# Performance work log

Hardware: AMD Instinct MI355X
Metric: run time of the kernel (lower is better)

Reference implementation:

```python
import jax, jax.numpy as jnp
import numpy as np

B, T, C = 4, 2048, 1024
H = 16
D = C // H  # 64

def setup_inputs() -> dict:
    key = jax.random.key(0)
    k1, k2, k3, k4, k5 = jax.random.split(key, 5)
    s = 0.02
    return {
        "x": jax.random.normal(k1, (B, T, C), dtype=jnp.float32),
        "Wqkv": jax.random.normal(k2, (C, 3 * C), dtype=jnp.float32) * s,
        "bqkv": jnp.zeros((3 * C,), dtype=jnp.float32),
        "Wout": jax.random.normal(k3, (C, C), dtype=jnp.float32) * s,
        "bout": jnp.zeros((C,), dtype=jnp.float32),
    }

def reference(x, Wqkv, bqkv, Wout, bout):
    b, t, c = x.shape
    scale = D ** -0.5
    qkv = x @ Wqkv + bqkv                      # [B,T,3C]
    qkv = qkv.reshape(b, t, 3, H, D)
    q = qkv[:, :, 0].transpose(0, 2, 1, 3)     # [B,H,T,D]
    k = qkv[:, :, 1].transpose(0, 2, 1, 3)
    v = qkv[:, :, 2].transpose(0, 2, 1, 3)
    att = jnp.einsum('bhqd,bhkd->bhqk', q, k) * scale
    causal = jnp.tril(jnp.ones((t, t), dtype=bool))
    att = jnp.where(causal, att, -jnp.inf)
    att = jax.nn.softmax(att, axis=-1)
    y = jnp.einsum('bhqk,bhkd->bhqd', att, v)  # [B,H,T,D]
    y = y.transpose(0, 2, 1, 3).reshape(b, t, c)
    return y @ Wout + bout
```

## Files before the change

kernel.cpp:

```cpp
#include <hip/hip_runtime.h>
#include <hip/hip_bf16.h>


using f32x4 = __attribute__((ext_vector_type(4))) float;
using s16x8 = __attribute__((ext_vector_type(8))) short;
using s16x4 = __attribute__((ext_vector_type(4))) short;

#define MFMA16(a, b, c) __builtin_amdgcn_mfma_f32_16x16x32_bf16(a, b, c, 0, 0, 0)

__device__ __forceinline__ unsigned short f2bf(float f) {
    unsigned u = __builtin_bit_cast(unsigned, f);
    u += 0x7fffu + ((u >> 16) & 1u);
    return (unsigned short)(u >> 16);
}

__device__ __forceinline__ void gl_lds16(const void* g, void* l) {
    __builtin_amdgcn_global_load_lds(
        (const __attribute__((address_space(1))) void*)g,
        (__attribute__((address_space(3))) void*)l, 16, 0, 0);
}

#define VMCNT(N) asm volatile("s_waitcnt vmcnt(" #N ")" ::: "memory")
#define RBAR()   __builtin_amdgcn_s_barrier()

__global__ __launch_bounds__(256) void cvt_x(const float* __restrict__ x,
                                             unsigned short* __restrict__ xb, int n4) {
    int i = blockIdx.x * 256 + threadIdx.x;
    if (i < n4) {
        f32x4 v = ((const f32x4*)x)[i];
        s16x4 o;
        o[0] = (short)f2bf(v[0]); o[1] = (short)f2bf(v[1]);
        o[2] = (short)f2bf(v[2]); o[3] = (short)f2bf(v[3]);
        ((s16x4*)xb)[i] = o;
    }
}

__global__ __launch_bounds__(256) void cvt_tr(const float* __restrict__ W,
                                              unsigned short* __restrict__ Wt,
                                              int R, int Cc) {
    __shared__ unsigned short tile[64][72];
    const int r0 = blockIdx.x * 64, c0 = blockIdx.y * 64;
    const int tid = threadIdx.x;
    const int r = tid >> 4, c4 = (tid & 15) * 4;
#pragma unroll
    for (int i = 0; i < 4; ++i) {
        f32x4 v = *(const f32x4*)(W + (size_t)(r0 + r + i * 16) * Cc + c0 + c4);
#pragma unroll
        for (int j = 0; j < 4; ++j) tile[r + i * 16][c4 + j] = f2bf(v[j]);
    }
    __syncthreads();
#pragma unroll
    for (int i = 0; i < 4; ++i) {
        s16x4 o;
#pragma unroll
        for (int j = 0; j < 4; ++j) o[j] = (short)tile[c4 + j][r + i * 16];
        *(s16x4*)(Wt + (size_t)(c0 + r + i * 16) * R + r0 + c4) = o;
    }
}

template <int MODE>
__global__ __launch_bounds__(256, 2) void gemm_bt(
    const unsigned short* __restrict__ A, const unsigned short* __restrict__ Bt,
    const float* __restrict__ bias,
    unsigned short* __restrict__ qp, unsigned short* __restrict__ kp,
    unsigned short* __restrict__ vtp, float* __restrict__ outp,
    int M, int N, int K)
{
    __shared__ unsigned short As[2][128 * 64];
    __shared__ unsigned short Bs[2][128 * 64];

    const int tid  = threadIdx.x;
    const int lane = tid & 63, w = tid >> 6;
    const int wm = w >> 1, wn = w & 1;
    const int g = lane >> 4, li = lane & 15;
    const int m0 = blockIdx.x * 128, n0 = blockIdx.y * 128;

    const int srow = lane >> 3;
    const int ssw  = ((lane & 7) ^ srow) * 8;

    f32x4 acc[4][4] = {};

    auto STAGE = [&](int buf, int k0) {
#pragma unroll
        for (int j = 0; j < 4; ++j) {
            const int rr = w * 32 + j * 8;
            gl_lds16(A  + (size_t)(m0 + rr + srow) * K + k0 + ssw, &As[buf][rr * 64]);
            gl_lds16(Bt + (size_t)(n0 + rr + srow) * K + k0 + ssw, &Bs[buf][rr * 64]);
        }
    };

    STAGE(0, 0);
    VMCNT(0);
    __syncthreads();

    const int nt = K >> 6;
    int cur = 0;
    for (int t = 0; t < nt; ++t) {
        if (t + 1 < nt) STAGE(cur ^ 1, (t + 1) << 6);

        s16x8 af[4][2], bf[4][2];
#pragma unroll
        for (int i = 0; i < 4; ++i) {
            const int ra = wm * 64 + i * 16 + li;
            const int rb = wn * 64 + i * 16 + li;
#pragma unroll
            for (int kk = 0; kk < 2; ++kk) {
                af[i][kk] = *(const s16x8*)(
                    &As[cur][ra * 64 + (((kk * 4 + g) ^ (ra & 7)) << 3)]);
                bf[i][kk] = *(const s16x8*)(
                    &Bs[cur][rb * 64 + (((kk * 4 + g) ^ (rb & 7)) << 3)]);
            }
        }

        __builtin_amdgcn_s_setprio(1);
#pragma unroll
        for (int kk = 0; kk < 2; ++kk)
#pragma unroll
            for (int mi = 0; mi < 4; ++mi)
#pragma unroll
                for (int ni = 0; ni < 4; ++ni)
                    acc[mi][ni] = MFMA16(af[mi][kk], bf[ni][kk], acc[mi][ni]);
        __builtin_amdgcn_s_setprio(0);

        VMCNT(0);
        __syncthreads();
        cur ^= 1;
    }

#pragma unroll
    for (int ni = 0; ni < 4; ++ni) {
        const int n = n0 + wn * 64 + ni * 16 + li;
        const float bv = bias[n];
        const int s = n >> 10, h = (n >> 6) & 15, d = n & 63;
#pragma unroll
        for (int mi = 0; mi < 4; ++mi) {
            const int mB = m0 + wm * 64 + mi * 16 + g * 4;
            float v0 = acc[mi][ni][0] + bv, v1 = acc[mi][ni][1] + bv;
            float v2 = acc[mi][ni][2] + bv, v3 = acc[mi][ni][3] + bv;
            if (MODE == 0) {
                const int b = mB >> 11, tt = mB & 2047;
                if (s == 2) {
                    unsigned pk01, pk23;
                    asm("v_cvt_pk_bf16_f32 %0, %1, %2" : "=v"(pk01) : "v"(v0), "v"(v1));
                    asm("v_cvt_pk_bf16_f32 %0, %1, %2" : "=v"(pk23) : "v"(v2), "v"(v3));
                    unsigned short* dst = vtp + ((size_t)(b * 16 + h) * 64 + d) * 2048 + tt;
                    *(unsigned*)dst = pk01;
                    *(unsigned*)(dst + 2) = pk23;
                } else {
                    const float sc2 = (s == 0) ? 0.1803368801111143f : 1.0f;
                    unsigned short* dst =
                        ((s == 0) ? qp : kp) + ((size_t)(b * 16 + h) * 2048 + tt) * 64 + d;
                    dst[0]   = f2bf(v0 * sc2);
                    dst[64]  = f2bf(v1 * sc2);
                    dst[128] = f2bf(v2 * sc2);
                    dst[192] = f2bf(v3 * sc2);
                }
            } else {
                float* dst = outp + (size_t)mB * N + n;
                dst[0] = v0; dst[N] = v1; dst[2 * N] = v2; dst[3 * N] = v3;
            }
        }
    }
}

__device__ __forceinline__ void qk_softmax(
    const unsigned short* Ks, const s16x8 qf0, const s16x8 qf1,
    f32x4 (&O)[4], float& m, float& l,
    unsigned short (*Psw)[72], s16x8& pf0, s16x8& pf1,
    int kbase, int wq0, int qrow, int g, int li)
{
    f32x4 sT[4];
    __builtin_amdgcn_s_setprio(1);
#pragma unroll
    for (int nf = 0; nf < 4; ++nf) {
        const int r = nf * 16 + li;
        s16x8 kf0 = *(const s16x8*)(Ks + r * 64 + ((g ^ (li & 7)) << 3));
        s16x8 kf1 = *(const s16x8*)(Ks + r * 64 + (((g + 4) ^ (li & 7)) << 3));
        f32x4 a = {};
        a = MFMA16(kf0, qf0, a);
        a = MFMA16(kf1, qf1, a);
        sT[nf] = a;
    }
    __builtin_amdgcn_s_setprio(0);

    if (kbase + 63 > wq0) {
#pragma unroll
        for (int nf = 0; nf < 4; ++nf)
#pragma unroll
            for (int r = 0; r < 4; ++r)
                if (kbase + nf * 16 + g * 4 + r > qrow) sT[nf][r] = -1e30f;
    }

    float t0 = fmaxf(fmaxf(sT[0][0], sT[0][1]), sT[0][2]);
    float t1 = fmaxf(fmaxf(sT[0][3], sT[1][0]), sT[1][1]);
    float t2 = fmaxf(fmaxf(sT[1][2], sT[1][3]), sT[2][0]);
    float t3 = fmaxf(fmaxf(sT[2][1], sT[2][2]), sT[2][3]);
    float t4 = fmaxf(fmaxf(sT[3][0], sT[3][1]), sT[3][2]);
    float mx = fmaxf(fmaxf(t0, t1), t2);
    mx = fmaxf(fmaxf(mx, t3), fmaxf(t4, sT[3][3]));
    mx = fmaxf(mx, __shfl_xor(mx, 16));
    mx = fmaxf(mx, __shfl_xor(mx, 32));

    if (__any(mx > m + 8.f)) {
        const float mnew = fmaxf(m, mx);
        const float fac  = __builtin_amdgcn_exp2f(m - mnew);
        m = mnew;
        l *= fac;
        float facr[4];
#pragma unroll
        for (int r = 0; r < 4; ++r) facr[r] = __shfl(fac, g * 4 + r);
#pragma unroll
        for (int nf = 0; nf < 4; ++nf)
#pragma unroll
            for (int r = 0; r < 4; ++r) O[nf][r] *= facr[r];
    }

    float rs = 0.f;
#pragma unroll
    for (int nf = 0; nf < 4; ++nf)
#pragma unroll
        for (int r = 0; r < 4; ++r) {
            float p = __builtin_amdgcn_exp2f(sT[nf][r] - m);
            sT[nf][r] = p;
            rs += p;
        }
    rs += __shfl_xor(rs, 16);
    rs += __shfl_xor(rs, 32);
    l += rs;

#pragma unroll
    for (int nf = 0; nf < 4; ++nf) {
        unsigned pk0, pk1;
        asm("v_cvt_pk_bf16_f32 %0, %1, %2" : "=v"(pk0) : "v"(sT[nf][0]), "v"(sT[nf][1]));
        asm("v_cvt_pk_bf16_f32 %0, %1, %2" : "=v"(pk1) : "v"(sT[nf][2]), "v"(sT[nf][3]));
        uint2 pv; pv.x = pk0; pv.y = pk1;
        *(uint2*)(&Psw[li][nf * 16 + g * 4]) = pv;
    }
    pf0 = *(const s16x8*)(&Psw[li][g * 8]);
    pf1 = *(const s16x8*)(&Psw[li][32 + g * 8]);
}

__global__ __launch_bounds__(256, 4) void attn_k(
    const unsigned short* __restrict__ qbuf,
    const unsigned short* __restrict__ kbuf,
    const unsigned short* __restrict__ vtbuf,
    unsigned short* __restrict__ ybuf)
{
    __shared__ unsigned short Ks[2][4096];
    __shared__ unsigned short Vs[4096];
    __shared__ unsigned short Ps[4][16][72];

    const int tid  = threadIdx.x;
    const int lane = tid & 63, w = tid >> 6;
    const int g = lane >> 4, li = lane & 15;

    const int id   = blockIdx.x;
    const int slot = id >> 3;
    const int bh   = (id & 7) * 8 + (slot & 7);
    const int bx   = slot >> 3;
    const int qtA  = 31 - bx, qtB = bx;

    const unsigned short* qb  = qbuf  + (size_t)bh * 131072;
    const unsigned short* kb  = kbuf  + (size_t)bh * 131072;
    const unsigned short* vtb = vtbuf + (size_t)bh * 131072;
    const int b = bh >> 4, h = bh & 15;

    const int srow = lane >> 3;
    const int ssw  = ((lane & 7) ^ srow) * 8;

    auto STAGE_K = [&](int buf, int kbase) {
#pragma unroll
        for (int jj = 0; jj < 2; ++jj) {
            const int j = w * 2 + jj, row = j * 8 + srow;
            gl_lds16(kb + (size_t)(kbase + row) * 64 + ssw, &Ks[buf][j * 512]);
        }
    };
    auto STAGE_V = [&](int kbase) {
#pragma unroll
        for (int jj = 0; jj < 2; ++jj) {
            const int j = w * 2 + jj, row = j * 8 + srow;
            gl_lds16(vtb + (size_t)row * 2048 + kbase + ssw, &Vs[j * 512]);
        }
    };

    const int wqA = qtA * 64 + w * 16, qrowA = wqA + li;
    const int wqB = qtB * 64 + w * 16, qrowB = wqB + li;

    const unsigned short* qrA = qb + (size_t)qrowA * 64 + g * 8;
    const s16x8 qfA0 = *(const s16x8*)qrA;
    const s16x8 qfA1 = *(const s16x8*)(qrA + 32);
    const unsigned short* qrB = qb + (size_t)qrowB * 64 + g * 8;
    const s16x8 qfB0 = *(const s16x8*)qrB;
    const s16x8 qfB1 = *(const s16x8*)(qrB + 32);

    f32x4 OA[4] = {}, OB[4] = {};
    float mA = -1e30f, lA = 0.f, mB = -1e30f, lB = 0.f;

    const int nkb = qtA + 1;
    STAGE_K(0, 0);
    STAGE_V(0);
    VMCNT(0);
    RBAR();

    int bK = 0;
    for (int t = 0; t < nkb; ++t) {
        const int kbase = t * 64;
        const bool actB = (t <= qtB);
        const bool more = (t + 1 < nkb);

        if (more) {
            STAGE_K(bK ^ 1, kbase + 64);
            VMCNT(4);
        } else {
            VMCNT(2);
        }
        RBAR();

        s16x8 pfA0, pfA1, pfB0, pfB1;
        qk_softmax(&Ks[bK][0], qfA0, qfA1, OA, mA, lA, &Ps[w][0], pfA0, pfA1,
                   kbase, wqA, qrowA, g, li);
        if (actB)
            qk_softmax(&Ks[bK][0], qfB0, qfB1, OB, mB, lB, &Ps[w][0], pfB0, pfB1,
                       kbase, wqB, qrowB, g, li);

        if (more) VMCNT(2); else VMCNT(0);
        RBAR();

        __builtin_amdgcn_s_setprio(1);
#pragma unroll
        for (int nf = 0; nf < 4; ++nf) {
            const int d = nf * 16 + li;
            s16x8 vf0 = *(const s16x8*)(Vs + d * 64 + ((g ^ (li & 7)) << 3));
            s16x8 vf1 = *(const s16x8*)(Vs + d * 64 + (((g + 4) ^ (li & 7)) << 3));
            OA[nf] = MFMA16(pfA0, vf0, OA[nf]);
            OA[nf] = MFMA16(pfA1, vf1, OA[nf]);
            if (actB) {
                OB[nf] = MFMA16(pfB0, vf0, OB[nf]);
                OB[nf] = MFMA16(pfB1, vf1, OB[nf]);
            }
        }
        __builtin_amdgcn_s_setprio(0);

        if (more) {
            RBAR();
            STAGE_V(kbase + 64);
        }
        bK ^= 1;
    }

    {
        const float linv = __builtin_amdgcn_rcpf(lA);
        float lr[4];
#pragma unroll
        for (int r = 0; r < 4; ++r) lr[r] = __shfl(linv, g * 4 + r);
#pragma unroll
        for (int nf = 0; nf < 4; ++nf)
#pragma unroll
            for (int r = 0; r < 4; ++r) {
                const int row = wqA + g * 4 + r;
                ybuf[((size_t)(b * 2048 + row)) * 1024 + h * 64 + nf * 16 + li] =
                    f2bf(OA[nf][r] * lr[r]);
            }
    }
    {
        const float linv = __builtin_amdgcn_rcpf(lB);
        float lr[4];
#pragma unroll
        for (int r = 0; r < 4; ++r) lr[r] = __shfl(linv, g * 4 + r);
#pragma unroll
        for (int nf = 0; nf < 4; ++nf)
#pragma unroll
            for (int r = 0; r < 4; ++r) {
                const int row = wqB + g * 4 + r;
                ybuf[((size_t)(b * 2048 + row)) * 1024 + h * 64 + nf * 16 + li] =
                    f2bf(OB[nf][r] * lr[r]);
            }
    }
}

extern "C" void kernel_launch(void* const* d_in, const int* in_sizes, int n_in,
                              void* d_out, int out_size, void* d_ws, size_t ws_size,
                              hipStream_t stream)
{
    const float* x    = (const float*)d_in[0];
    const float* Wqkv = (const float*)d_in[1];
    const float* bqkv = (const float*)d_in[2];
    const float* Wout = (const float*)d_in[3];
    const float* bout = (const float*)d_in[4];

    unsigned short* ws0 = (unsigned short*)d_ws;
    unsigned short* ws1 = ws0 + (size_t)8388608;
    unsigned short* ws2 = ws0 + (size_t)2 * 8388608;
    unsigned short* ws3 = ws0 + (size_t)3 * 8388608;

    unsigned short* xbf   = (unsigned short*)d_out;
    unsigned short* WqkvT = xbf + (size_t)8388608;

    cvt_x<<<8192, 256, 0, stream>>>(x, xbf, 2097152);
    cvt_tr<<<dim3(16, 48), 256, 0, stream>>>(Wqkv, WqkvT, 1024, 3072);
    gemm_bt<0><<<dim3(64, 24), 256, 0, stream>>>(
        xbf, WqkvT, bqkv, ws0, ws1, ws2, nullptr, 8192, 3072, 1024);
    attn_k<<<1024, 256, 0, stream>>>(ws0, ws1, ws2, ws3);
    cvt_tr<<<dim3(16, 16), 256, 0, stream>>>(Wout, ws0, 1024, 1024);
    gemm_bt<1><<<dim3(64, 8), 256, 0, stream>>>(
        ws3, ws0, bout, nullptr, nullptr, nullptr, (float*)d_out, 8192, 1024, 1024);
}
```

Before: 170.9 us.

## Double-buffer V tile alongside K and drop mid-iteration barrier in attention

Adds a second V buffer in LDS so K and V for the next tile are prefetched together, removing the separate barrier between QK/softmax and PV and the late V staging. QK scores for both query tiles are interleaved in one MFMA loop sharing K fragment loads. The P scratch buffer switches from padded rows to an XOR-swizzled 64-wide layout to avoid bank conflicts while saving LDS. LDS use rises, which may affect occupancy at 4 blocks per CU.

```diff
diff --git a/kernel.cpp b/kernel.cpp
--- a/kernel.cpp
+++ b/kernel.cpp
@@ -163,26 +163,11 @@
     }
 }
 
-__device__ __forceinline__ void qk_softmax(
-    const unsigned short* Ks, const s16x8 qf0, const s16x8 qf1,
-    f32x4 (&O)[4], float& m, float& l,
-    unsigned short (*Psw)[72], s16x8& pf0, s16x8& pf1,
+__device__ __forceinline__ void softmax_pack(
+    f32x4 (&sT)[4], f32x4 (&O)[4], float& m, float& l,
+    char* PsRow, s16x8& pf0, s16x8& pf1,
     int kbase, int wq0, int qrow, int g, int li)
 {
-    f32x4 sT[4];
-    __builtin_amdgcn_s_setprio(1);
-#pragma unroll
-    for (int nf = 0; nf < 4; ++nf) {
-        const int r = nf * 16 + li;
-        s16x8 kf0 = *(const s16x8*)(Ks + r * 64 + ((g ^ (li & 7)) << 3));
-        s16x8 kf1 = *(const s16x8*)(Ks + r * 64 + (((g + 4) ^ (li & 7)) << 3));
-        f32x4 a = {};
-        a = MFMA16(kf0, qf0, a);
-        a = MFMA16(kf1, qf1, a);
-        sT[nf] = a;
-    }
-    __builtin_amdgcn_s_setprio(0);
-
     if (kbase + 63 > wq0) {
 #pragma unroll
         for (int nf = 0; nf < 4; ++nf)
@@ -228,16 +213,18 @@
     rs += __shfl_xor(rs, 32);
     l += rs;
 
+    const int swz = (li & 7) << 4;
+    char* rowp = PsRow + li * 128;
 #pragma unroll
     for (int nf = 0; nf < 4; ++nf) {
         unsigned pk0, pk1;
         asm("v_cvt_pk_bf16_f32 %0, %1, %2" : "=v"(pk0) : "v"(sT[nf][0]), "v"(sT[nf][1]));
         asm("v_cvt_pk_bf16_f32 %0, %1, %2" : "=v"(pk1) : "v"(sT[nf][2]), "v"(sT[nf][3]));
         uint2 pv; pv.x = pk0; pv.y = pk1;
-        *(uint2*)(&Psw[li][nf * 16 + g * 4]) = pv;
-    }
-    pf0 = *(const s16x8*)(&Psw[li][g * 8]);
-    pf1 = *(const s16x8*)(&Psw[li][32 + g * 8]);
+        *(uint2*)(rowp + ((nf * 32 + g * 8) ^ swz)) = pv;
+    }
+    pf0 = *(const s16x8*)(rowp + ((g * 16) ^ swz));
+    pf1 = *(const s16x8*)(rowp + ((64 + g * 16) ^ swz));
 }
 
 __global__ __launch_bounds__(256, 4) void attn_k(
@@ -247,8 +234,8 @@
     unsigned short* __restrict__ ybuf)
 {
     __shared__ unsigned short Ks[2][4096];
-    __shared__ unsigned short Vs[4096];
-    __shared__ unsigned short Ps[4][16][72];
+    __shared__ unsigned short Vs[2][4096];
+    __shared__ unsigned short Ps[4][16][64];
 
     const int tid  = threadIdx.x;
     const int lane = tid & 63, w = tid >> 6;
@@ -268,18 +255,12 @@
     const int srow = lane >> 3;
     const int ssw  = ((lane & 7) ^ srow) * 8;
 
-    auto STAGE_K = [&](int buf, int kbase) {
+    auto STAGE = [&](int p, int kbase) {
 #pragma unroll
         for (int jj = 0; jj < 2; ++jj) {
             const int j = w * 2 + jj, row = j * 8 + srow;
-            gl_lds16(kb + (size_t)(kbase + row) * 64 + ssw, &Ks[buf][j * 512]);
-        }
-    };
-    auto STAGE_V = [&](int kbase) {
-#pragma unroll
-        for (int jj = 0; jj < 2; ++jj) {
-            const int j = w * 2 + jj, row = j * 8 + srow;
-            gl_lds16(vtb + (size_t)row * 2048 + kbase + ssw, &Vs[j * 512]);
+            gl_lds16(kb  + (size_t)(kbase + row) * 64 + ssw, &Ks[p][j * 512]);
+            gl_lds16(vtb + (size_t)row * 2048 + kbase + ssw, &Vs[p][j * 512]);
         }
     };
 
@@ -297,41 +278,57 @@
     float mA = -1e30f, lA = 0.f, mB = -1e30f, lB = 0.f;
 
     const int nkb = qtA + 1;
-    STAGE_K(0, 0);
-    STAGE_V(0);
-    VMCNT(0);
-    RBAR();
-
-    int bK = 0;
+    STAGE(0, 0);
+
     for (int t = 0; t < nkb; ++t) {
+        const int p = t & 1;
         const int kbase = t * 64;
         const bool actB = (t <= qtB);
         const bool more = (t + 1 < nkb);
 
         if (more) {
-            STAGE_K(bK ^ 1, kbase + 64);
+            STAGE(p ^ 1, kbase + 64);
             VMCNT(4);
         } else {
-            VMCNT(2);
+            VMCNT(0);
         }
         RBAR();
 
+        f32x4 sA[4], sB[4];
+        __builtin_amdgcn_s_setprio(1);
+#pragma unroll
+        for (int nf = 0; nf < 4; ++nf) {
+            const int r = nf * 16 + li;
+            const unsigned short* Kp = &Ks[p][r * 64];
+            s16x8 kf0 = *(const s16x8*)(Kp + ((g ^ (li & 7)) << 3));
+            s16x8 kf1 = *(const s16x8*)(Kp + (((g + 4) ^ (li & 7)) << 3));
+            f32x4 a = {};
+            a = MFMA16(kf0, qfA0, a);
+            a = MFMA16(kf1, qfA1, a);
+            sA[nf] = a;
+            f32x4 bb = {};
+            if (actB) {
+                bb = MFMA16(kf0, qfB0, bb);
+                bb = MFMA16(kf1, qfB1, bb);
+            }
+            sB[nf] = bb;
+        }
+        __builtin_amdgcn_s_setprio(0);
+
         s16x8 pfA0, pfA1, pfB0, pfB1;
-        qk_softmax(&Ks[bK][0], qfA0, qfA1, OA, mA, lA, &Ps[w][0], pfA0, pfA1,
-                   kbase, wqA, qrowA, g, li);
+        softmax_pack(sA, OA, mA, lA, (char*)&Ps[w][0][0], pfA0, pfA1,
+                     kbase, wqA, qrowA, g, li);
         if (actB)
-            qk_softmax(&Ks[bK][0], qfB0, qfB1, OB, mB, lB, &Ps[w][0], pfB0, pfB1,
-                       kbase, wqB, qrowB, g, li);
-
-        if (more) VMCNT(2); else VMCNT(0);
-        RBAR();
+            softmax_pack(sB, OB, mB, lB, (char*)&Ps[w][0][0], pfB0, pfB1,
+                         kbase, wqB, qrowB, g, li);
 
         __builtin_amdgcn_s_setprio(1);
 #pragma unroll
         for (int nf = 0; nf < 4; ++nf) {
             const int d = nf * 16 + li;
-            s16x8 vf0 = *(const s16x8*)(Vs + d * 64 + ((g ^ (li & 7)) << 3));
-            s16x8 vf1 = *(const s16x8*)(Vs + d * 64 + (((g + 4) ^ (li & 7)) << 3));
+            const unsigned short* Vp = &Vs[p][d * 64];
+            s16x8 vf0 = *(const s16x8*)(Vp + ((g ^ (li & 7)) << 3));
+            s16x8 vf1 = *(const s16x8*)(Vp + (((g + 4) ^ (li & 7)) << 3));
             OA[nf] = MFMA16(pfA0, vf0, OA[nf]);
             OA[nf] = MFMA16(pfA1, vf1, OA[nf]);
             if (actB) {
@@ -341,11 +338,7 @@
         }
         __builtin_amdgcn_s_setprio(0);
 
-        if (more) {
-            RBAR();
-            STAGE_V(kbase + 64);
-        }
-        bK ^= 1;
+        if (more) RBAR();
     }
 
     {
```

Result: no change. 169.7 us (-0.7%).
